# Kernel optimization log

Hardware: AMD Instinct MI355X
Metric: run time of the kernel (lower is better)

The kernel has to match this reference:

```python
import jax, jax.numpy as jnp
import numpy as np

B, S, D, H = 2, 2048, 1024, 16
HD = D // H  # head_dim = 64
ROPE_BASE = 10000.0
NEG = -1e9


def rope_cos_sin(seq_len, head_dim, dtype):
    inv_freq = 1.0 / (ROPE_BASE ** (jnp.arange(0, head_dim, 2, dtype=jnp.float32) / head_dim))
    t = jnp.arange(seq_len, dtype=jnp.float32)
    freqs = jnp.outer(t, inv_freq)              # [S, HD/2]
    emb = jnp.concatenate([freqs, freqs], axis=-1)  # [S, HD]
    return jnp.cos(emb).astype(dtype), jnp.sin(emb).astype(dtype)


def rotate_half(x):
    half = x.shape[-1] // 2
    return jnp.concatenate([-x[..., half:], x[..., :half]], axis=-1)


def setup_inputs() -> dict:
    key = jax.random.key(0)
    ks = jax.random.split(key, 9)
    s = 0.02
    x = jax.random.normal(ks[0], (B, S, D), dtype=jnp.float32)
    # additive causal mask: 0 on/below diagonal, -1e9 above
    mask = jnp.where(jnp.tril(jnp.ones((S, S), dtype=bool)), 0.0, NEG).astype(jnp.float32)
    params = {
        'Wq': jax.random.normal(ks[1], (D, D), jnp.float32) * s,
        'bq': jnp.zeros((D,), jnp.float32),
        'Wk': jax.random.normal(ks[2], (D, D), jnp.float32) * s,
        'bk': jnp.zeros((D,), jnp.float32),
        'Wv': jax.random.normal(ks[3], (D, D), jnp.float32) * s,
        'bv': jnp.zeros((D,), jnp.float32),
        'Wo': jax.random.normal(ks[4], (D, D), jnp.float32) * s,
        'bo': jnp.zeros((D,), jnp.float32),
    }
    return {'x': x, 'mask': mask, **params}


def reference(x, mask, Wq, bq, Wk, bk, Wv, bv, Wo, bo):
    Bv, Sv, Dv = x.shape
    q = (x @ Wq + bq).reshape(Bv, Sv, H, HD).transpose(0, 2, 1, 3)  # [B,H,S,HD]
    k = (x @ Wk + bk).reshape(Bv, Sv, H, HD).transpose(0, 2, 1, 3)
    v = (x @ Wv + bv).reshape(Bv, Sv, H, HD).transpose(0, 2, 1, 3)
    cos, sin = rope_cos_sin(Sv, HD, x.dtype)      # [S, HD]
    cos = cos[None, None]                          # [1,1,S,HD]
    sin = sin[None, None]
    q = q * cos + rotate_half(q) * sin
    k = k * cos + rotate_half(k) * sin
    scale = jnp.asarray(np.sqrt(HD), x.dtype)
    scores = jnp.einsum('bhqd,bhkd->bhqk', q, k) / scale  # [B,H,S,S]
    scores = scores + mask[None, None]
    attn = jax.nn.softmax(scores, axis=-1)
    out = jnp.einsum('bhqk,bhkd->bhqd', attn, v)   # [B,H,S,HD]
    out = out.transpose(0, 2, 1, 3).reshape(Bv, Sv, Dv)
    return out @ Wo + bo
```

## Files before the change

### kernel.cpp

```cpp
#include <hip/hip_runtime.h>
#include <hip/hip_bf16.h>
#include <cstdint>

typedef __bf16 bf16;
typedef __bf16 bf16x4 __attribute__((ext_vector_type(4)));
typedef __bf16 bf16x8 __attribute__((ext_vector_type(8)));
typedef float f32x4 __attribute__((ext_vector_type(4)));

#define DEV __device__ __forceinline__

DEV void gl_lds16(const void* g, void* l) {
    __builtin_amdgcn_global_load_lds(
        (__attribute__((address_space(1))) void*)(uintptr_t)g,
        (__attribute__((address_space(3))) void*)(uint32_t)(uintptr_t)l,
        16, 0, 0);
}

DEV f32x4 mfma16(bf16x8 a, bf16x8 b, f32x4 c) {
    return __builtin_amdgcn_mfma_f32_16x16x32_bf16(a, b, c, 0, 0, 0);
}

__global__ __launch_bounds__(256) void prep_k(
    const float* __restrict__ x, bf16* __restrict__ xb,
    const float* __restrict__ w0, const float* __restrict__ w1,
    const float* __restrict__ w2, const float* __restrict__ w3,
    bf16* __restrict__ WT, float* __restrict__ cosT, float* __restrict__ sinT) {
    __shared__ float t[32][33];
    const int blk = (int)blockIdx.x;
    const int tid = threadIdx.x;
    if (blk < 4096) {
        const int i = blk * 256 + tid;
        const float4 v = ((const float4*)x)[i];
        bf16x4 o = {(bf16)v.x, (bf16)v.y, (bf16)v.z, (bf16)v.w};
        *(bf16x4*)(xb + (size_t)i * 4) = o;
    } else if (blk < 8192) {
        const int j = blk - 4096;
        const int z = j >> 10, jy = (j >> 5) & 31, jx = j & 31;
        const float* W = z == 0 ? w0 : z == 1 ? w1 : z == 2 ? w2 : w3;
        bf16* dst = WT + (size_t)z * 1024 * 1024;
        const int tx = tid & 31, ty = tid >> 5;
        const int kb = jx * 32, nb = jy * 32;
#pragma unroll
        for (int i = 0; i < 4; ++i)
            t[ty + i * 8][tx] = W[(size_t)(kb + ty + i * 8) * 1024 + nb + tx];
        __syncthreads();
#pragma unroll
        for (int i = 0; i < 4; ++i)
            dst[(size_t)(nb + ty + i * 8) * 1024 + kb + tx] = (bf16)t[tx][ty + i * 8];
    } else {
        const int tt = (blk - 8192) * 256 + tid;
        const int s = tt >> 6, i = tt & 31;
        const float inv = expf(-(float)i * (9.210340371976184f / 32.0f));
        const float ang = (float)s * inv;
        cosT[tt] = cosf(ang);
        sinT[tt] = sinf(ang);
    }
}

__global__ __launch_bounds__(512, 4) void gemm256_k(
    const bf16* __restrict__ A, const bf16* __restrict__ BT,
    const float* __restrict__ bq, const float* __restrict__ bk,
    const float* __restrict__ bv,
    bf16* __restrict__ outQ, bf16* __restrict__ outK, bf16* __restrict__ outV,
    const float* __restrict__ cosT, const float* __restrict__ sinT) {
    extern __shared__ char smem[];
    const int tid = threadIdx.x;
    const int lane = tid & 63, wv = tid >> 6;
    const int wm2 = wv >> 2, wn2 = wv & 3;
    const int q = lane & 15, g = lane >> 4;

    const int gid = (int)blockIdx.x;
    const int xcd = gid & 7, idx = gid >> 3;
    const int bm = (xcd & 3) * 8 + (idx & 7);
    const int bn = (xcd >> 2) * 6 + (idx >> 3);

    const bf16* Ab = A + (size_t)bm * 128 * 1024;
    const bf16* Bb = BT + (size_t)bn * 256 * 1024;

    auto stage = [&](int b, int kb) {
        char* base = smem + b * 24576;
        {
            const int Xs = tid * 16;
            const int row = Xs >> 6;
            const int cb = (Xs & 63) ^ ((row & 3) << 4);
            gl_lds16(Ab + (size_t)row * 1024 + kb + (cb >> 1), base + Xs);
        }
#pragma unroll
        for (int i = 0; i < 2; ++i) {
            const int Xs = i * 8192 + tid * 16;
            const int row = Xs >> 6;
            const int cb = (Xs & 63) ^ ((row & 3) << 4);
            gl_lds16(Bb + (size_t)row * 1024 + kb + (cb >> 1), base + 8192 + Xs);
        }
    };

    f32x4 acc[4][4] = {};
    const int swz = (q & 3) << 4;

    stage(0, 0);

    for (int t = 0; t < 32; ++t) {
        asm volatile("s_waitcnt vmcnt(0)" ::: "memory");
        __builtin_amdgcn_s_barrier();
        if (t + 1 < 32) stage((t + 1) & 1, (t + 1) * 32);
        const char* cbuf = smem + (t & 1) * 24576;
        bf16x8 af[4], bfr[4];
#pragma unroll
        for (int ni = 0; ni < 4; ++ni) {
            const int row = wn2 * 64 + ni * 16 + q;
            bfr[ni] = *(const bf16x8*)(cbuf + 8192 + row * 64 + ((g * 16) ^ swz));
        }
#pragma unroll
        for (int j = 0; j < 4; ++j) {
            const int row = wm2 * 64 + j * 16 + q;
            af[j] = *(const bf16x8*)(cbuf + row * 64 + ((g * 16) ^ swz));
        }
        __builtin_amdgcn_s_setprio(1);
#pragma unroll
        for (int j = 0; j < 4; ++j)
#pragma unroll
            for (int ni = 0; ni < 4; ++ni)
                acc[j][ni] = mfma16(af[j], bfr[ni], acc[j][ni]);
        __builtin_amdgcn_s_setprio(0);
    }

    const int n0 = bn * 256 + wn2 * 64;
    const int seg = n0 >> 10;
    const int nloc = n0 & 1023;
    const int h = nloc >> 6;
    const float* bias = seg == 0 ? bq : (seg == 1 ? bk : bv);
    const float qsc = (seg == 0) ? 0.125f : 1.0f;
    float bvv[4];
#pragma unroll
    for (int ni = 0; ni < 4; ++ni) bvv[ni] = bias[nloc + ni * 16 + q];

    if (seg < 2) {
        bf16* dst = seg == 0 ? outQ : outK;
#pragma unroll
        for (int mi = 0; mi < 4; ++mi) {
#pragma unroll
            for (int r = 0; r < 4; ++r) {
                const int m = bm * 128 + wm2 * 64 + mi * 16 + g * 4 + r;
                const int s = m & 2047, bb = m >> 11;
                const size_t rowb = ((size_t)((bb << 4) | h) * 2048 + s) * 64;
#pragma unroll
                for (int ni = 0; ni < 4; ++ni) {
                    const int hd = ni * 16 + q;
                    const float c = cosT[s * 64 + hd], sn = sinT[s * 64 + hd];
                    const float v0 = acc[mi][ni][r] + bvv[ni];
                    const float v1 = acc[mi][ni ^ 2][r] + bvv[ni ^ 2];
                    dst[rowb + hd] = (bf16)((v0 * c + (ni < 2 ? -v1 : v1) * sn) * qsc);
                }
            }
        }
    } else {
        const int bb = (bm * 128) >> 11;
        bf16* vbase = outV + (size_t)((bb << 4) | h) * (64 * 2048);
        const int s0 = ((bm * 128) & 2047) + wm2 * 64;
#pragma unroll
        for (int rnd = 0; rnd < 2; ++rnd) {
            __builtin_amdgcn_s_barrier();
            if ((wv >> 2) == rnd) {
                bf16* Tw = (bf16*)smem + (wv & 3) * (64 * 72);
#pragma unroll
                for (int mi2 = 0; mi2 < 4; ++mi2)
#pragma unroll
                    for (int ni = 0; ni < 4; ++ni)
#pragma unroll
                        for (int r = 0; r < 4; ++r)
                            Tw[(ni * 16 + q) * 72 + mi2 * 16 + g * 4 + r] =
                                (bf16)(acc[mi2][ni][r] + bvv[ni]);
#pragma unroll
                for (int i = 0; i < 8; ++i) {
                    const int row = i * 8 + (lane >> 3);
                    const int col = (lane & 7) * 8;
                    bf16x8 vvv = *(const bf16x8*)(Tw + row * 72 + col);
                    *(bf16x8*)(vbase + (size_t)row * 2048 + s0 + col) = vvv;
                }
            }
        }
    }
}

__global__ __launch_bounds__(256) void gemmo_k(
    const bf16* __restrict__ A, const bf16* __restrict__ BT,
    const float* __restrict__ bias0, float* __restrict__ outF) {
    extern __shared__ char smem[];
    const int tid = threadIdx.x;
    const int lane = tid & 63;
    const int wv = tid >> 6;
    const int wm = wv >> 1, wn = wv & 1;
    const int bm = blockIdx.x, bn = blockIdx.y;
    const int q = lane & 15, g = lane >> 4;

    const bf16* Ab = A + (size_t)bm * 128 * 1024;
    const bf16* Bb = BT + (size_t)bn * 128 * 1024;
    const int r0 = tid >> 2, c0 = (tid & 3) * 8;

    auto stage = [&](int b, int kb) {
        char* base = smem + b * 16384;
        gl_lds16(Ab + (size_t)r0 * 1024 + kb + c0, base + tid * 16);
        gl_lds16(Ab + (size_t)(r0 + 64) * 1024 + kb + c0, base + 4096 + tid * 16);
        gl_lds16(Bb + (size_t)r0 * 1024 + kb + c0, base + 8192 + tid * 16);
        gl_lds16(Bb + (size_t)(r0 + 64) * 1024 + kb + c0, base + 12288 + tid * 16);
    };

    f32x4 acc[4][4] = {};

    stage(0, 0);
    stage(1, 32);
    asm volatile("s_waitcnt vmcnt(4)" ::: "memory");
    __builtin_amdgcn_s_barrier();

    for (int kt = 0; kt < 32; ++kt) {
        if (kt + 2 < 32) stage((kt + 2) % 3, (kt + 2) * 32);
        const bf16* As = (const bf16*)(smem + (kt % 3) * 16384);
        const bf16* Bs = As + 128 * 32;
        bf16x8 af[4], bfr[4];
#pragma unroll
        for (int mi = 0; mi < 4; ++mi)
            af[mi] = *(const bf16x8*)(As + (wm * 64 + mi * 16 + q) * 32 + g * 8);
#pragma unroll
        for (int ni = 0; ni < 4; ++ni)
            bfr[ni] = *(const bf16x8*)(Bs + (wn * 64 + ni * 16 + q) * 32 + g * 8);
#pragma unroll
        for (int mi = 0; mi < 4; ++mi)
#pragma unroll
            for (int ni = 0; ni < 4; ++ni)
                acc[mi][ni] = mfma16(af[mi], bfr[ni], acc[mi][ni]);
        if (kt + 2 < 32) asm volatile("s_waitcnt vmcnt(4)" ::: "memory");
        else             asm volatile("s_waitcnt vmcnt(0)" ::: "memory");
        __builtin_amdgcn_s_barrier();
    }

    const int n0 = bn * 128 + wn * 64;
    float bvv[4];
#pragma unroll
    for (int ni = 0; ni < 4; ++ni) bvv[ni] = bias0[n0 + ni * 16 + q];
#pragma unroll
    for (int mi = 0; mi < 4; ++mi)
#pragma unroll
        for (int r = 0; r < 4; ++r) {
            const int m = bm * 128 + wm * 64 + mi * 16 + g * 4 + r;
#pragma unroll
            for (int ni = 0; ni < 4; ++ni)
                outF[(size_t)m * 1024 + n0 + ni * 16 + q] = acc[mi][ni][r] + bvv[ni];
        }
}

__global__ __launch_bounds__(512, 2) void attn_k(const bf16* __restrict__ Qr,
                                                 const bf16* __restrict__ Kr,
                                                 const bf16* __restrict__ Vt,
                                                 bf16* __restrict__ AO) {
    const int gid = (int)blockIdx.x;
    const int xcd = gid & 7;
    const int bh = xcd + 8 * ((gid >> 3) & 3);
    const int idx = gid >> 5;
    const int p = idx >> 1;
    const int h = 1 - (idx & 1);
    const int tid = threadIdx.x;
    const int lane = tid & 63, wv = tid >> 6;
    const int q = lane & 15, g = lane >> 4;
    const int qt_w = (wv >> 2) ? p : (15 - p);
    const int q0w = qt_w * 128 + h * 64 + (wv & 3) * 16;
    const int nt = 31 - 2 * p + h;
    const size_t hb = (size_t)bh * (2048 * 64);
    extern __shared__ char smem[];
    bf16* P = (bf16*)(smem + 49152 + wv * 2304);

    const bf16* Kg = Kr + hb;
    const bf16* Vg = Vt + hb;
    const int swz = (q & 7) << 4;

    auto stage = [&](int b, int kb) {
        char* base = smem + b * 16384;
        {
            const int X = tid * 16;
            const int row = X >> 7;
            const int cbg = (X & 127) ^ ((row & 7) << 4);
            gl_lds16(Kg + (size_t)(kb + row) * 64 + (cbg >> 1), base + X);
        }
        {
            const int X = tid * 16;
            const int row = X >> 7;
            const int cbg = (X & 127) ^ ((row & 7) << 4);
            gl_lds16(Vg + (size_t)row * 2048 + kb + (cbg >> 1), base + 8192 + X);
        }
    };

    bf16x8 qf[2];
    {
        const bf16* qp = Qr + hb + (size_t)(q0w + q) * 64 + g * 8;
        qf[0] = *(const bf16x8*)(qp);
        qf[1] = *(const bf16x8*)(qp + 32);
    }
    f32x4 o[4] = {};
    float l_run = 0.0f;
    const f32x4 z4 = {0.f, 0.f, 0.f, 0.f};
    const int rmax = q0w + 15;

    stage(0, 0);
    stage(1, 64);
    asm volatile("s_waitcnt vmcnt(2)" ::: "memory");
    __builtin_amdgcn_s_barrier();

    for (int kt = 0; kt < nt; ++kt) {
        const int kb = kt * 64;
        if (kt + 2 < nt) stage((kt + 2) % 3, kb + 128);
        if (kb <= rmax) {
            char* Kl = smem + (kt % 3) * 16384;
            char* Vl = Kl + 8192;
            f32x4 st[4];
            __builtin_amdgcn_s_setprio(1);
#pragma unroll
            for (int f = 0; f < 4; ++f) {
                const int row = f * 16 + q;
                const bf16x8 k0 = *(const bf16x8*)(Kl + row * 128 + ((g * 16) ^ swz));
                const bf16x8 k1 = *(const bf16x8*)(Kl + row * 128 + ((64 + g * 16) ^ swz));
                f32x4 t0 = mfma16(k0, qf[0], z4);
                st[f] = mfma16(k1, qf[1], t0);
            }
            __builtin_amdgcn_s_setprio(0);
            bf16x8 vf[4][2];
#pragma unroll
            for (int nf = 0; nf < 4; ++nf) {
                const int row = nf * 16 + q;
                vf[nf][0] = *(const bf16x8*)(Vl + row * 128 + ((g * 16) ^ swz));
                vf[nf][1] = *(const bf16x8*)(Vl + row * 128 + ((64 + g * 16) ^ swz));
            }
            float tsum = 0.f;
            if (kb + 63 > q0w) {
#pragma unroll
                for (int f = 0; f < 4; ++f)
#pragma unroll
                    for (int r = 0; r < 4; ++r) {
                        float sv = st[f][r];
                        if (kb + f * 16 + g * 4 + r > q0w + q) sv = -3.0e38f;
                        const float pv = __expf(sv);
                        st[f][r] = pv;
                        tsum += pv;
                    }
            } else {
#pragma unroll
                for (int f = 0; f < 4; ++f)
#pragma unroll
                    for (int r = 0; r < 4; ++r) {
                        const float pv = __expf(st[f][r]);
                        st[f][r] = pv;
                        tsum += pv;
                    }
            }
            l_run += tsum;
#pragma unroll
            for (int f = 0; f < 4; ++f) {
                bf16x4 pv = {(bf16)st[f][0], (bf16)st[f][1],
                             (bf16)st[f][2], (bf16)st[f][3]};
                *(bf16x4*)&P[q * 72 + f * 16 + g * 4] = pv;
            }
            __builtin_amdgcn_s_setprio(1);
#pragma unroll
            for (int t = 0; t < 2; ++t) {
                const bf16x8 pa = *(const bf16x8*)&P[q * 72 + t * 32 + g * 8];
#pragma unroll
                for (int nf = 0; nf < 4; ++nf)
                    o[nf] = mfma16(pa, vf[nf][t], o[nf]);
            }
            __builtin_amdgcn_s_setprio(0);
        }
        if (kt + 2 < nt) asm volatile("s_waitcnt vmcnt(2)" ::: "memory");
        else             asm volatile("s_waitcnt vmcnt(0)" ::: "memory");
        __builtin_amdgcn_s_barrier();
    }

    l_run += __shfl_xor(l_run, 16);
    l_run += __shfl_xor(l_run, 32);
    float li[4];
#pragma unroll
    for (int r = 0; r < 4; ++r) li[r] = 1.0f / __shfl(l_run, g * 4 + r);
    const int b_ = bh >> 4, h_ = bh & 15;
#pragma unroll
    for (int nf = 0; nf < 4; ++nf)
#pragma unroll
        for (int r = 0; r < 4; ++r) {
            const int qg = q0w + g * 4 + r;
            AO[(size_t)(b_ * 2048 + qg) * 1024 + h_ * 64 + nf * 16 + q] =
                (bf16)(o[nf][r] * li[r]);
        }
}


extern "C" void kernel_launch(void* const* d_in, const int* in_sizes, int n_in,
                              void* d_out, int out_size, void* d_ws, size_t ws_size,
                              hipStream_t stream) {
    const float* x  = (const float*)d_in[0];
    const float* Wq = (const float*)d_in[2];
    const float* bq = (const float*)d_in[3];
    const float* Wk = (const float*)d_in[4];
    const float* bk = (const float*)d_in[5];
    const float* Wv = (const float*)d_in[6];
    const float* bv = (const float*)d_in[7];
    const float* Wo = (const float*)d_in[8];
    const float* bo = (const float*)d_in[9];
    float* out = (float*)d_out;
    char* ws = (char*)d_ws;
    const size_t MB_ = 1024 * 1024;
    bf16* xb    = (bf16*)(ws);
    bf16* WT    = (bf16*)(ws + 8 * MB_);
    bf16* Qrp   = (bf16*)(ws + 16 * MB_);
    bf16* Krp   = (bf16*)(ws + 24 * MB_);
    bf16* Vt    = (bf16*)(ws + 32 * MB_);
    bf16* AO    = (bf16*)(ws + 40 * MB_);
    float* cosT = (float*)(ws + 48 * MB_);
    float* sinT = (float*)(ws + 48 * MB_ + 512 * 1024);

    prep_k<<<8704, 256, 0, stream>>>(x, xb, Wq, Wk, Wv, Wo, WT, cosT, sinT);
    gemm256_k<<<dim3(384), 512, 49152, stream>>>(xb, WT, bq, bk, bv,
                                                 Qrp, Krp, Vt, cosT, sinT);
    attn_k<<<dim3(512, 1), 512, 67584, stream>>>(Qrp, Krp, Vt, AO);
    gemmo_k<<<dim3(32, 8), 256, 49152, stream>>>(AO, WT + (size_t)3072 * 1024, bo, out);
}
```

Before: 95.83 us.

## Retile output-projection GEMM to 64x128 with swizzled LDS and priority hints

The output-projection GEMM now uses 64x128 tiles instead of 128x128, which doubles the grid to 512 blocks for better occupancy on the many CUs, and adds launch bounds for two blocks per CU. Each wave owns a 64x32 slice. LDS staging uses an XOR swizzle on 16-byte chunks to reduce bank conflicts on fragment reads. MFMA sections are wrapped in s_setprio. In exchange, smaller tiles cut operand reuse and raise total global traffic for the B matrix.

```diff
diff --git a/kernel.cpp b/kernel.cpp
--- a/kernel.cpp
+++ b/kernel.cpp
@@ -182,68 +182,81 @@
     }
 }
 
-__global__ __launch_bounds__(256) void gemmo_k(
+__global__ __launch_bounds__(256, 2) void gemmo_k(
     const bf16* __restrict__ A, const bf16* __restrict__ BT,
     const float* __restrict__ bias0, float* __restrict__ outF) {
     extern __shared__ char smem[];
     const int tid = threadIdx.x;
     const int lane = tid & 63;
     const int wv = tid >> 6;
-    const int wm = wv >> 1, wn = wv & 1;
     const int bm = blockIdx.x, bn = blockIdx.y;
     const int q = lane & 15, g = lane >> 4;
 
-    const bf16* Ab = A + (size_t)bm * 128 * 1024;
+    const bf16* Ab = A + (size_t)bm * 64 * 1024;
     const bf16* Bb = BT + (size_t)bn * 128 * 1024;
-    const int r0 = tid >> 2, c0 = (tid & 3) * 8;
 
     auto stage = [&](int b, int kb) {
-        char* base = smem + b * 16384;
-        gl_lds16(Ab + (size_t)r0 * 1024 + kb + c0, base + tid * 16);
-        gl_lds16(Ab + (size_t)(r0 + 64) * 1024 + kb + c0, base + 4096 + tid * 16);
-        gl_lds16(Bb + (size_t)r0 * 1024 + kb + c0, base + 8192 + tid * 16);
-        gl_lds16(Bb + (size_t)(r0 + 64) * 1024 + kb + c0, base + 12288 + tid * 16);
+        char* base = smem + b * 12288;
+        {
+            const int Xs = tid * 16;
+            const int row = Xs >> 6;
+            const int cb = (Xs & 63) ^ ((row & 3) << 4);
+            gl_lds16(Ab + (size_t)row * 1024 + kb + (cb >> 1), base + Xs);
+        }
+#pragma unroll
+        for (int i = 0; i < 2; ++i) {
+            const int Xs = i * 4096 + tid * 16;
+            const int row = Xs >> 6;
+            const int cb = (Xs & 63) ^ ((row & 3) << 4);
+            gl_lds16(Bb + (size_t)row * 1024 + kb + (cb >> 1), base + 4096 + Xs);
+        }
     };
 
-    f32x4 acc[4][4] = {};
+    f32x4 acc[4][2] = {};
+    const int swz = (q & 3) << 4;
 
     stage(0, 0);
     stage(1, 32);
-    asm volatile("s_waitcnt vmcnt(4)" ::: "memory");
+    asm volatile("s_waitcnt vmcnt(3)" ::: "memory");
     __builtin_amdgcn_s_barrier();
 
     for (int kt = 0; kt < 32; ++kt) {
         if (kt + 2 < 32) stage((kt + 2) % 3, (kt + 2) * 32);
-        const bf16* As = (const bf16*)(smem + (kt % 3) * 16384);
-        const bf16* Bs = As + 128 * 32;
-        bf16x8 af[4], bfr[4];
+        const char* cbuf = smem + (kt % 3) * 12288;
+        bf16x8 af[4], bfr[2];
+#pragma unroll
+        for (int mi = 0; mi < 4; ++mi) {
+            const int row = mi * 16 + q;
+            af[mi] = *(const bf16x8*)(cbuf + row * 64 + ((g * 16) ^ swz));
+        }
+#pragma unroll
+        for (int ni = 0; ni < 2; ++ni) {
+            const int row = wv * 32 + ni * 16 + q;
+            bfr[ni] = *(const bf16x8*)(cbuf + 4096 + row * 64 + ((g * 16) ^ swz));
+        }
+        __builtin_amdgcn_s_setprio(1);
 #pragma unroll
         for (int mi = 0; mi < 4; ++mi)
-            af[mi] = *(const bf16x8*)(As + (wm * 64 + mi * 16 + q) * 32 + g * 8);
-#pragma unroll
-        for (int ni = 0; ni < 4; ++ni)
-            bfr[ni] = *(const bf16x8*)(Bs + (wn * 64 + ni * 16 + q) * 32 + g * 8);
-#pragma unroll
-        for (int mi = 0; mi < 4; ++mi)
-#pragma unroll
-            for (int ni = 0; ni < 4; ++ni)
+#pragma unroll
+            for (int ni = 0; ni < 2; ++ni)
                 acc[mi][ni] = mfma16(af[mi], bfr[ni], acc[mi][ni]);
-        if (kt + 2 < 32) asm volatile("s_waitcnt vmcnt(4)" ::: "memory");
+        __builtin_amdgcn_s_setprio(0);
+        if (kt + 2 < 32) asm volatile("s_waitcnt vmcnt(3)" ::: "memory");
         else             asm volatile("s_waitcnt vmcnt(0)" ::: "memory");
         __builtin_amdgcn_s_barrier();
     }
 
-    const int n0 = bn * 128 + wn * 64;
-    float bvv[4];
-#pragma unroll
-    for (int ni = 0; ni < 4; ++ni) bvv[ni] = bias0[n0 + ni * 16 + q];
+    const int n0 = bn * 128 + wv * 32;
+    float bvv[2];
+#pragma unroll
+    for (int ni = 0; ni < 2; ++ni) bvv[ni] = bias0[n0 + ni * 16 + q];
 #pragma unroll
     for (int mi = 0; mi < 4; ++mi)
 #pragma unroll
         for (int r = 0; r < 4; ++r) {
-            const int m = bm * 128 + wm * 64 + mi * 16 + g * 4 + r;
-#pragma unroll
-            for (int ni = 0; ni < 4; ++ni)
+            const int m = bm * 64 + mi * 16 + g * 4 + r;
+#pragma unroll
+            for (int ni = 0; ni < 2; ++ni)
                 outF[(size_t)m * 1024 + n0 + ni * 16 + q] = acc[mi][ni][r] + bvv[ni];
         }
 }
@@ -417,5 +430,5 @@
     gemm256_k<<<dim3(384), 512, 49152, stream>>>(xb, WT, bq, bk, bv,
                                                  Qrp, Krp, Vt, cosT, sinT);
     attn_k<<<dim3(512, 1), 512, 67584, stream>>>(Qrp, Krp, Vt, AO);
-    gemmo_k<<<dim3(32, 8), 256, 49152, stream>>>(AO, WT + (size_t)3072 * 1024, bo, out);
-}
+    gemmo_k<<<dim3(64, 8), 256, 36864, stream>>>(AO, WT + (size_t)3072 * 1024, bo, out);
+}
```

Result: no change. 94.56 us, median of 2 (-1.3%).
